# Optimization experiments

Measured on AMD Instinct MI355X. Metric: run time of the kernel, lower is better.

## Reference

```python
import jax, jax.numpy as jnp
import numpy as np

N_NODES = 20000
N_EDGES = 320000
N_GRAPHS = 32
C = 256
L = 4
IN_DIM = 739
EDGE_DIM = 2 * C + 6
LN_EPS = 1e-5


def _layernorm(x, g, b):
    mu = jnp.mean(x, axis=-1, keepdims=True)
    var = jnp.mean(jnp.square(x - mu), axis=-1, keepdims=True)
    return (x - mu) * jax.lax.rsqrt(var + LN_EPS) * g + b


def setup_inputs() -> dict:
    key = jax.random.key(0)
    ks = jax.random.split(key, 20)
    d = {}
    d["x"] = jax.random.normal(ks[0], (N_NODES, IN_DIM), jnp.float32)
    d["x_pos"] = jax.random.normal(ks[1], (N_NODES, 3), jnp.float32)
    d["edge_index"] = jax.random.randint(ks[2], (2, N_EDGES), 0, N_NODES, jnp.int32)
    d["batch"] = jnp.sort(jax.random.randint(ks[3], (N_NODES,), 0, N_GRAPHS, jnp.int32))
    s = 0.02
    d["dense_w"] = jax.random.normal(ks[4], (IN_DIM, C), jnp.float32) * s
    d["dense_b"] = jnp.zeros((C,), jnp.float32)
    d["d1_w"] = jax.random.normal(ks[5], (L, C, C), jnp.float32) * s
    d["d1_b"] = jnp.zeros((L, C), jnp.float32)
    d["ln1_g"] = jnp.ones((L, EDGE_DIM), jnp.float32)
    d["ln1_b"] = jnp.zeros((L, EDGE_DIM), jnp.float32)
    d["w1_w"] = jax.random.normal(ks[6], (L, EDGE_DIM, 4), jnp.float32) * s
    d["w1_b"] = jnp.zeros((L, 4), jnp.float32)
    d["ln2_g"] = jnp.ones((L, 4), jnp.float32)
    d["ln2_b"] = jnp.zeros((L, 4), jnp.float32)
    d["w2_w"] = jax.random.normal(ks[7], (L, 4, 1), jnp.float32) * s
    d["w2_b"] = jnp.zeros((L, 1), jnp.float32)
    d["d2_w"] = jax.random.normal(ks[8], (L, C, C), jnp.float32) * s
    d["d2_b"] = jnp.zeros((L, C), jnp.float32)
    d["head_w"] = jax.random.normal(ks[9], (C, 1), jnp.float32) * s
    d["head_b"] = jnp.zeros((1,), jnp.float32)
    return d


def reference(x, x_pos, edge_index, batch, dense_w, dense_b, d1_w, d1_b,
              ln1_g, ln1_b, w1_w, w1_b, ln2_g, ln2_b, w2_w, w2_b,
              d2_w, d2_b, head_w, head_b):
    n = x.shape[0]
    src, dst = edge_index[0], edge_index[1]
    h = x @ dense_w + dense_b  # [N, C]
    for l in range(d1_w.shape[0]):
        # message: dense1 -> GELU (dropout is identity in eval)
        m = jax.nn.gelu(h @ d1_w[l] + d1_b[l], approximate=False)  # [N, C]
        sx = m[src]                                                # [E, C]
        # edge-MLP input: [src_x, dst_x, src_pos, dst_pos]
        e = jnp.concatenate([sx, m[dst], x_pos[src], x_pos[dst]], axis=-1)  # [E, 2C+6]
        e = _layernorm(e, ln1_g[l], ln1_b[l])
        e = jax.nn.gelu(e @ w1_w[l] + w1_b[l], approximate=False)  # [E, 4]
        e = _layernorm(e, ln2_g[l], ln2_b[l])
        w = jax.nn.sigmoid(e @ w2_w[l] + w2_b[l])                  # [E, 1]
        agg = jax.ops.segment_sum(sx * w, dst, num_segments=n)     # [N, C]
        # update: dense2 -> GELU
        h = jax.nn.gelu(agg @ d2_w[l] + d2_b[l], approximate=False)
    # global mean pool over graphs
    sums = jax.ops.segment_sum(h, batch, num_segments=N_GRAPHS)           # [G, C]
    cnts = jax.ops.segment_sum(jnp.ones((n, 1), h.dtype), batch, num_segments=N_GRAPHS)
    pooled = sums / jnp.maximum(cnts, 1.0)
    return pooled @ head_w + head_b  # [G, 1]
```

## Files before the change

### kernel.cpp

```cpp
#include <hip/hip_runtime.h>
#include <math.h>

#define N_NODES 20000
#define N_EDGES 320000
#define N_GRAPHS 32
#define CDIM 256
#define IN_DIMV 739
#define KPAD_DENSE 768
#define ED_DIM 518
#define NLAYERS 4
#define LN_EPS 1e-5f
#define SCAN_BLOCKS ((N_NODES + 255) / 256)

typedef _Float16 f16x8 __attribute__((ext_vector_type(8)));
typedef _Float16 f16x4 __attribute__((ext_vector_type(4)));
typedef float f32x4 __attribute__((ext_vector_type(4)));

__device__ __forceinline__ float gelu_exact(float x) {
    return 0.5f * x * (1.f + erff(x * 0.7071067811865475f));
}

__global__ __launch_bounds__(256)
void prep_all(const float* __restrict__ ln1_g, const float* __restrict__ ln1_b,
              const float* __restrict__ w1_w, float* __restrict__ cw,
              float* __restrict__ SgSb,
              const float* __restrict__ dense_w, _Float16* __restrict__ wt_dense,
              const float* __restrict__ d1_w, const float* __restrict__ d2_w,
              _Float16* __restrict__ wt_sq, int* __restrict__ deg,
              float* __restrict__ sdot) {
    __shared__ float smem[2048 + 64];
    int b = blockIdx.x, tid = threadIdx.x;
    if (b < 79) {
        int i = b * 256 + tid;
        if (i < N_NODES) deg[i] = 0;
    } else if (b < 83) {
        int l = b - 79;
        float sg[4] = {0, 0, 0, 0}, sb[4] = {0, 0, 0, 0};
        for (int i = tid; i < ED_DIM; i += 256) {
            float g = ln1_g[l * ED_DIM + i];
            float bb = ln1_b[l * ED_DIM + i];
            float4 w = *(const float4*)&w1_w[(size_t)(l * ED_DIM + i) * 4];
            float4 c = make_float4(g * w.x, g * w.y, g * w.z, g * w.w);
            *(float4*)&cw[(size_t)(l * ED_DIM + i) * 4] = c;
            sg[0] += c.x; sg[1] += c.y; sg[2] += c.z; sg[3] += c.w;
            sb[0] += bb * w.x; sb[1] += bb * w.y; sb[2] += bb * w.z; sb[3] += bb * w.w;
        }
        for (int c = 0; c < 4; c++) { smem[tid * 8 + c] = sg[c]; smem[tid * 8 + 4 + c] = sb[c]; }
        __syncthreads();
        for (int s = 128; s > 0; s >>= 1) {
            if (tid < s)
                for (int c = 0; c < 8; c++) smem[tid * 8 + c] += smem[(tid + s) * 8 + c];
            __syncthreads();
        }
        if (tid < 8) SgSb[l * 8 + tid] = smem[tid];
    } else if (b < 275) {
        int q = b - 83;
        int kt = q >> 3, nt = q & 7;
        int i = tid >> 5, j = tid & 31;
        float* T = smem;
#pragma unroll
        for (int ii = 0; ii < 4; ii++) {
            int k = kt * 32 + i + ii * 8;
            T[(i + ii * 8) * 33 + j] = (k < IN_DIMV) ? dense_w[(size_t)k * 256 + nt * 32 + j] : 0.f;
        }
        __syncthreads();
#pragma unroll
        for (int ii = 0; ii < 4; ii++) {
            int n = nt * 32 + i + ii * 8;
            wt_dense[(size_t)n * KPAD_DENSE + kt * 32 + j] = (_Float16)T[j * 33 + i + ii * 8];
        }
    } else if (b < 787) {
        int q = b - 275;
        int z = q >> 6, kt = (q >> 3) & 7, nt = q & 7;
        const float* W = (z < 4) ? d1_w + (size_t)z * 65536 : d2_w + (size_t)(z - 4) * 65536;
        _Float16* O = wt_sq + (size_t)z * 65536;
        int i = tid >> 5, j = tid & 31;
        float* T = smem;
#pragma unroll
        for (int ii = 0; ii < 4; ii++)
            T[(i + ii * 8) * 33 + j] = W[(size_t)(kt * 32 + i + ii * 8) * 256 + nt * 32 + j];
        __syncthreads();
#pragma unroll
        for (int ii = 0; ii < 4; ii++)
            O[(size_t)(nt * 32 + i + ii * 8) * 256 + kt * 32 + j] = (_Float16)T[j * 33 + i + ii * 8];
    } else {
        int i = (b - 787) * 256 + tid;
        if (i < N_NODES) sdot[i] = 0.f;
    }
}

__global__ void hist_gstart_kernel(const int* __restrict__ ei, const int* __restrict__ batch,
                                   int* __restrict__ deg, int* __restrict__ gstart) {
    int e = blockIdx.x * 256 + threadIdx.x;
    if (e < N_EDGES) atomicAdd(&deg[ei[N_EDGES + e]], 1);
    if (e < N_NODES) {
        int b = batch[e];
        int bprev = (e == 0) ? -1 : batch[e - 1];
        for (int g = bprev + 1; g <= b; g++) gstart[g] = e;
        if (e == N_NODES - 1)
            for (int g = b + 1; g <= N_GRAPHS; g++) gstart[g] = N_NODES;
    }
}

__global__ __launch_bounds__(256)
void scan1_kernel(const int* __restrict__ deg, int* __restrict__ bsum) {
    __shared__ int red[256];
    int t = threadIdx.x;
    int i = blockIdx.x * 256 + t;
    red[t] = (i < N_NODES) ? deg[i] : 0;
    __syncthreads();
    for (int s = 128; s > 0; s >>= 1) {
        if (t < s) red[t] += red[t + s];
        __syncthreads();
    }
    if (t == 0) bsum[blockIdx.x] = red[0];
}

__global__ __launch_bounds__(128)
void scan2_kernel(const int* __restrict__ bsum, int* __restrict__ boff) {
    __shared__ int s[128];
    int t = threadIdx.x;
    int v = (t < SCAN_BLOCKS) ? bsum[t] : 0;
    s[t] = v;
    __syncthreads();
    for (int off = 1; off < 128; off <<= 1) {
        int o = (t >= off) ? s[t - off] : 0;
        __syncthreads();
        s[t] += o;
        __syncthreads();
    }
    if (t < SCAN_BLOCKS) boff[t] = s[t] - v;
}

__global__ __launch_bounds__(256)
void scan3_kernel(const int* __restrict__ deg, const int* __restrict__ boff,
                  int* __restrict__ row_start, int* __restrict__ cursor) {
    __shared__ int s[256];
    int t = threadIdx.x;
    int i = blockIdx.x * 256 + t;
    int v = (i < N_NODES) ? deg[i] : 0;
    s[t] = v;
    __syncthreads();
    for (int off = 1; off < 256; off <<= 1) {
        int o = (t >= off) ? s[t - off] : 0;
        __syncthreads();
        s[t] += o;
        __syncthreads();
    }
    int base = boff[blockIdx.x];
    int excl = base + s[t] - v;
    if (i < N_NODES) {
        row_start[i] = excl;
        cursor[i] = excl;
    }
    if (i == N_NODES - 1) row_start[N_NODES] = base + s[t];
}

__global__ void scatter_kernel(const int* __restrict__ ei, int* __restrict__ cursor,
                               int* __restrict__ csr_src, int* __restrict__ slot) {
    int e = blockIdx.x * 256 + threadIdx.x;
    if (e < N_EDGES) {
        int d = ei[N_EDGES + e];
        int pos = atomicAdd(&cursor[d], 1);
        csr_src[pos] = ei[e];
        slot[e] = pos;
    }
}

__global__ __launch_bounds__(256)
void gemm_dense(const float* __restrict__ A, const _Float16* __restrict__ Bt,
                const float* __restrict__ bias, _Float16* __restrict__ C) {
    __shared__ __align__(16) _Float16 As[32 * 72];
    __shared__ __align__(16) _Float16 Bs[128 * 72];
    int tid = threadIdx.x;
    int row0 = blockIdx.x * 32;
    int col0 = blockIdx.y * 128;
    int wave = tid >> 6, lane = tid & 63;
    int quad = lane >> 4, lrow = lane & 15;
    int wrow = wave >> 1, wcol = wave & 1;

    int ar = tid >> 3, ak8 = (tid & 7) * 8;
    int br = tid >> 1, bh = (tid & 1) * 32;

    const float* Arow = &A[(size_t)(row0 + ar) * IN_DIMV];
    const _Float16* Brow = &Bt[(size_t)(col0 + br) * KPAD_DENSE];

    const int ntiles = KPAD_DENSE >> 6;
    float a_f[8];
#pragma unroll
    for (int j = 0; j < 8; j++) {
        int gk = ak8 + j;
        a_f[j] = (gk < IN_DIMV) ? Arow[gk] : 0.f;
    }
    uint4 b_raw0 = *(const uint4*)&Brow[bh];
    uint4 b_raw1 = *(const uint4*)&Brow[bh + 8];
    uint4 b_raw2 = *(const uint4*)&Brow[bh + 16];
    uint4 b_raw3 = *(const uint4*)&Brow[bh + 24];

    f32x4 acc[4];
#pragma unroll
    for (int t = 0; t < 4; t++) acc[t] = (f32x4){0.f, 0.f, 0.f, 0.f};

    for (int kt = 0; kt < ntiles; ++kt) {
        f16x8 ah;
#pragma unroll
        for (int j = 0; j < 8; j++) ah[j] = (_Float16)a_f[j];
        *(f16x8*)&As[ar * 72 + ak8] = ah;
        *(uint4*)&Bs[br * 72 + bh] = b_raw0;
        *(uint4*)&Bs[br * 72 + bh + 8] = b_raw1;
        *(uint4*)&Bs[br * 72 + bh + 16] = b_raw2;
        *(uint4*)&Bs[br * 72 + bh + 24] = b_raw3;
        __syncthreads();

        if (kt + 1 < ntiles) {
            int k0 = (kt + 1) << 6;
#pragma unroll
            for (int j = 0; j < 8; j++) {
                int gk = k0 + ak8 + j;
                a_f[j] = (gk < IN_DIMV) ? Arow[gk] : 0.f;
            }
            b_raw0 = *(const uint4*)&Brow[k0 + bh];
            b_raw1 = *(const uint4*)&Brow[k0 + bh + 8];
            b_raw2 = *(const uint4*)&Brow[k0 + bh + 16];
            b_raw3 = *(const uint4*)&Brow[k0 + bh + 24];
        }

#pragma unroll
        for (int h = 0; h < 2; h++) {
            f16x8 af = *(const f16x8*)&As[(wrow * 16 + lrow) * 72 + h * 32 + quad * 8];
#pragma unroll
            for (int t = 0; t < 4; t++) {
                f16x8 bf = *(const f16x8*)&Bs[((wcol * 4 + t) * 16 + lrow) * 72 + h * 32 + quad * 8];
                acc[t] = __builtin_amdgcn_mfma_f32_16x16x32_f16(af, bf, acc[t], 0, 0, 0);
            }
        }
        __syncthreads();
    }

    int orow = row0 + wrow * 16 + quad * 4;
#pragma unroll
    for (int t = 0; t < 4; t++) {
        int col = col0 + (wcol * 4 + t) * 16 + lrow;
        float bv = bias[col];
#pragma unroll
        for (int r = 0; r < 4; r++)
            C[(size_t)(orow + r) * 256 + col] = (_Float16)(acc[t][r] + bv);
    }
}

template <bool GELU, bool DOT>
__global__ __launch_bounds__(256)
void gemm_mfma(const _Float16* __restrict__ A, const _Float16* __restrict__ Bt,
               const float* __restrict__ bias, _Float16* __restrict__ C,
               const float* __restrict__ head_w, float* __restrict__ sdot) {
    __shared__ __align__(16) _Float16 As[32 * 72];
    __shared__ __align__(16) _Float16 Bs[128 * 72];
    int tid = threadIdx.x;
    int row0 = blockIdx.x * 32;
    int col0 = blockIdx.y * 128;
    int wave = tid >> 6, lane = tid & 63;
    int quad = lane >> 4, lrow = lane & 15;
    int wrow = wave >> 1, wcol = wave & 1;

    int ar = tid >> 3, ak8 = (tid & 7) * 8;
    int br = tid >> 1, bh = (tid & 1) * 32;

    const _Float16* Arow = &A[(size_t)(row0 + ar) * CDIM];
    const _Float16* Brow = &Bt[(size_t)(col0 + br) * CDIM];

    const int ntiles = CDIM >> 6;
    uint4 a_raw = *(const uint4*)&Arow[ak8];
    uint4 b_raw0 = *(const uint4*)&Brow[bh];
    uint4 b_raw1 = *(const uint4*)&Brow[bh + 8];
    uint4 b_raw2 = *(const uint4*)&Brow[bh + 16];
    uint4 b_raw3 = *(const uint4*)&Brow[bh + 24];

    f32x4 acc[4];
#pragma unroll
    for (int t = 0; t < 4; t++) acc[t] = (f32x4){0.f, 0.f, 0.f, 0.f};

    for (int kt = 0; kt < ntiles; ++kt) {
        *(uint4*)&As[ar * 72 + ak8] = a_raw;
        *(uint4*)&Bs[br * 72 + bh] = b_raw0;
        *(uint4*)&Bs[br * 72 + bh + 8] = b_raw1;
        *(uint4*)&Bs[br * 72 + bh + 16] = b_raw2;
        *(uint4*)&Bs[br * 72 + bh + 24] = b_raw3;
        __syncthreads();

        if (kt + 1 < ntiles) {
            int k0 = (kt + 1) << 6;
            a_raw = *(const uint4*)&Arow[k0 + ak8];
            b_raw0 = *(const uint4*)&Brow[k0 + bh];
            b_raw1 = *(const uint4*)&Brow[k0 + bh + 8];
            b_raw2 = *(const uint4*)&Brow[k0 + bh + 16];
            b_raw3 = *(const uint4*)&Brow[k0 + bh + 24];
        }

#pragma unroll
        for (int h = 0; h < 2; h++) {
            f16x8 af = *(const f16x8*)&As[(wrow * 16 + lrow) * 72 + h * 32 + quad * 8];
#pragma unroll
            for (int t = 0; t < 4; t++) {
                f16x8 bf = *(const f16x8*)&Bs[((wcol * 4 + t) * 16 + lrow) * 72 + h * 32 + quad * 8];
                acc[t] = __builtin_amdgcn_mfma_f32_16x16x32_f16(af, bf, acc[t], 0, 0, 0);
            }
        }
        __syncthreads();
    }

    int orow = row0 + wrow * 16 + quad * 4;
    if (DOT) {
        float dp[4] = {0.f, 0.f, 0.f, 0.f};
#pragma unroll
        for (int t = 0; t < 4; t++) {
            int col = col0 + (wcol * 4 + t) * 16 + lrow;
            float hw = head_w[col];
            float bv = bias[col];
#pragma unroll
            for (int r = 0; r < 4; r++)
                dp[r] += gelu_exact(acc[t][r] + bv) * hw;
        }
#pragma unroll
        for (int r = 0; r < 4; r++) {
#pragma unroll
            for (int off = 1; off < 16; off <<= 1)
                dp[r] += __shfl_xor(dp[r], off, 64);
        }
        if (lrow == 0) {
#pragma unroll
            for (int r = 0; r < 4; r++) atomicAdd(&sdot[orow + r], dp[r]);
        }
    } else {
#pragma unroll
        for (int t = 0; t < 4; t++) {
            int col = col0 + (wcol * 4 + t) * 16 + lrow;
            float bv = bias[col];
#pragma unroll
            for (int r = 0; r < 4; r++) {
                float v = acc[t][r] + bv;
                C[(size_t)(orow + r) * 256 + col] = (_Float16)(GELU ? gelu_exact(v) : v);
            }
        }
    }
}

__global__ __launch_bounds__(256)
void node_summary_kernel(const _Float16* __restrict__ m, const float* __restrict__ cw,
                         float* __restrict__ ns) {
    __shared__ __align__(16) float4 s_cw[512];
    int tid = threadIdx.x;
    for (int i = tid; i < 512; i += 256) s_cw[i] = *(const float4*)&cw[(size_t)i * 4];
    __syncthreads();
    int n = blockIdx.x * 4 + (tid >> 6);
    if (n >= N_NODES) return;
    int lane = tid & 63;
    f16x4 a4 = *(const f16x4*)&m[(size_t)n * CDIM + lane * 4];
    float av[4] = {(float)a4[0], (float)a4[1], (float)a4[2], (float)a4[3]};
    float Q1 = 0.f, Q2 = 0.f, P1[4] = {0, 0, 0, 0}, P2[4] = {0, 0, 0, 0};
#pragma unroll
    for (int j = 0; j < 4; j++) {
        Q1 += av[j];
        Q2 += av[j] * av[j];
        float4 c0 = s_cw[lane * 4 + j];
        float4 c1 = s_cw[256 + lane * 4 + j];
        P1[0] += av[j] * c0.x; P1[1] += av[j] * c0.y; P1[2] += av[j] * c0.z; P1[3] += av[j] * c0.w;
        P2[0] += av[j] * c1.x; P2[1] += av[j] * c1.y; P2[2] += av[j] * c1.z; P2[3] += av[j] * c1.w;
    }
#pragma unroll
    for (int off = 1; off < 64; off <<= 1) {
        Q1 += __shfl_xor(Q1, off, 64);
        Q2 += __shfl_xor(Q2, off, 64);
        P1[0] += __shfl_xor(P1[0], off, 64);
        P1[1] += __shfl_xor(P1[1], off, 64);
        P1[2] += __shfl_xor(P1[2], off, 64);
        P1[3] += __shfl_xor(P1[3], off, 64);
        P2[0] += __shfl_xor(P2[0], off, 64);
        P2[1] += __shfl_xor(P2[1], off, 64);
        P2[2] += __shfl_xor(P2[2], off, 64);
        P2[3] += __shfl_xor(P2[3], off, 64);
    }
    if (lane == 0) {
        float* p = &ns[(size_t)n * 12];
        *(float4*)p = make_float4(P1[0], P1[1], P1[2], P1[3]);
        *(float4*)(p + 4) = make_float4(P2[0], P2[1], P2[2], P2[3]);
        p[8] = Q1;
        p[9] = Q2;
    }
}

__global__ __launch_bounds__(256)
void edge_weight_kernel(const float* __restrict__ ns, const float* __restrict__ x_pos,
                        const int* __restrict__ ei, const float* __restrict__ cw,
                        const float* __restrict__ SgSb, const float* __restrict__ w1_b,
                        const float* __restrict__ ln2_g, const float* __restrict__ ln2_b,
                        const float* __restrict__ w2_w, const float* __restrict__ w2_b,
                        const int* __restrict__ slot, float* __restrict__ w_csr) {
    int e = blockIdx.x * 256 + threadIdx.x;
    if (e >= N_EDGES) return;
    int s = ei[e], d = ei[N_EDGES + e];
    const float* nss = &ns[(size_t)s * 12];
    const float* nsd = &ns[(size_t)d * 12];
    float4 p1 = *(const float4*)nss;
    float4 p2 = *(const float4*)(nsd + 4);
    float S1 = nss[8] + nsd[8];
    float S2 = nss[9] + nsd[9];
    float D[4] = {p1.x + p2.x, p1.y + p2.y, p1.z + p2.z, p1.w + p2.w};
    float ps[6];
    ps[0] = x_pos[(size_t)s * 3 + 0];
    ps[1] = x_pos[(size_t)s * 3 + 1];
    ps[2] = x_pos[(size_t)s * 3 + 2];
    ps[3] = x_pos[(size_t)d * 3 + 0];
    ps[4] = x_pos[(size_t)d * 3 + 1];
    ps[5] = x_pos[(size_t)d * 3 + 2];
#pragma unroll
    for (int k = 0; k < 6; k++) {
        S1 += ps[k];
        S2 += ps[k] * ps[k];
        float4 c = *(const float4*)&cw[(size_t)(512 + k) * 4];
        D[0] += ps[k] * c.x; D[1] += ps[k] * c.y; D[2] += ps[k] * c.z; D[3] += ps[k] * c.w;
    }
    const float inv = 1.f / 518.f;
    float mu = S1 * inv;
    float var = fmaf(-mu, mu, S2 * inv);
    float rstd = rsqrtf(var + LN_EPS);
    float t[4];
#pragma unroll
    for (int c = 0; c < 4; c++)
        t[c] = gelu_exact(rstd * (D[c] - mu * SgSb[c]) + SgSb[4 + c] + w1_b[c]);
    float mu2 = 0.25f * (t[0] + t[1] + t[2] + t[3]);
    float var2 = 0.25f * ((t[0] - mu2) * (t[0] - mu2) + (t[1] - mu2) * (t[1] - mu2) +
                          (t[2] - mu2) * (t[2] - mu2) + (t[3] - mu2) * (t[3] - mu2));
    float r2 = rsqrtf(var2 + LN_EPS);
    float z = w2_b[0];
#pragma unroll
    for (int c = 0; c < 4; c++)
        z += ((t[c] - mu2) * r2 * ln2_g[c] + ln2_b[c]) * w2_w[c];
    w_csr[slot[e]] = 1.f / (1.f + expf(-z));
}

__global__ __launch_bounds__(256)
void agg_kernel(const _Float16* __restrict__ m, const int* __restrict__ csr_src,
                const float* __restrict__ w_csr, const int* __restrict__ row_start,
                _Float16* __restrict__ agg) {
    int n = blockIdx.x * 4 + (threadIdx.x >> 6);
    if (n >= N_NODES) return;
    int lane = threadIdx.x & 63;
    int beg = row_start[n], end = row_start[n + 1];
    float a0 = 0.f, a1 = 0.f, a2 = 0.f, a3 = 0.f;
    int j = beg;
    for (; j + 8 <= end; j += 8) {
        int si[8];
        float wi[8];
#pragma unroll
        for (int u = 0; u < 8; u++) { si[u] = csr_src[j + u]; wi[u] = w_csr[j + u]; }
        f16x4 v[8];
#pragma unroll
        for (int u = 0; u < 8; u++) v[u] = *(const f16x4*)&m[(size_t)si[u] * CDIM + lane * 4];
#pragma unroll
        for (int u = 0; u < 8; u++) {
            a0 = fmaf(wi[u], (float)v[u][0], a0);
            a1 = fmaf(wi[u], (float)v[u][1], a1);
            a2 = fmaf(wi[u], (float)v[u][2], a2);
            a3 = fmaf(wi[u], (float)v[u][3], a3);
        }
    }
    for (; j < end; j++) {
        int s = csr_src[j];
        float w = w_csr[j];
        f16x4 v = *(const f16x4*)&m[(size_t)s * CDIM + lane * 4];
        a0 = fmaf(w, (float)v[0], a0);
        a1 = fmaf(w, (float)v[1], a1);
        a2 = fmaf(w, (float)v[2], a2);
        a3 = fmaf(w, (float)v[3], a3);
    }
    f16x4 o;
    o[0] = (_Float16)a0; o[1] = (_Float16)a1; o[2] = (_Float16)a2; o[3] = (_Float16)a3;
    *(f16x4*)&agg[(size_t)n * CDIM + lane * 4] = o;
}

__global__ __launch_bounds__(256)
void final_head_kernel(const float* __restrict__ sdot, const int* __restrict__ gstart,
                       const float* __restrict__ head_b, float* __restrict__ out) {
    int g = blockIdx.x;
    int t = threadIdx.x;
    int beg = gstart[g], end = gstart[g + 1];
    float s = 0.f;
    for (int i = beg + t; i < end; i += 256) s += sdot[i];
    __shared__ float red[256];
    red[t] = s;
    __syncthreads();
    for (int k = 128; k > 0; k >>= 1) {
        if (t < k) red[t] += red[t + k];
        __syncthreads();
    }
    if (t == 0) out[g] = red[0] / fmaxf((float)(end - beg), 1.f) + head_b[0];
}

extern "C" void kernel_launch(void* const* d_in, const int* in_sizes, int n_in,
                              void* d_out, int out_size, void* d_ws, size_t ws_size,
                              hipStream_t stream) {
    const float* x       = (const float*)d_in[0];
    const float* x_pos   = (const float*)d_in[1];
    const int*   ei      = (const int*)d_in[2];
    const int*   batch   = (const int*)d_in[3];
    const float* dense_w = (const float*)d_in[4];
    const float* dense_b = (const float*)d_in[5];
    const float* d1_w    = (const float*)d_in[6];
    const float* d1_b    = (const float*)d_in[7];
    const float* ln1_g   = (const float*)d_in[8];
    const float* ln1_b   = (const float*)d_in[9];
    const float* w1_w    = (const float*)d_in[10];
    const float* w1_b    = (const float*)d_in[11];
    const float* ln2_g   = (const float*)d_in[12];
    const float* ln2_b   = (const float*)d_in[13];
    const float* w2_w    = (const float*)d_in[14];
    const float* w2_b    = (const float*)d_in[15];
    const float* d2_w    = (const float*)d_in[16];
    const float* d2_b    = (const float*)d_in[17];
    const float* head_w  = (const float*)d_in[18];
    const float* head_b  = (const float*)d_in[19];
    float* out = (float*)d_out;

    _Float16* hbuf0 = (_Float16*)d_ws;
    _Float16* hbuf1 = hbuf0 + (size_t)N_NODES * CDIM;
    _Float16* wt_dense = hbuf1 + (size_t)N_NODES * CDIM;
    _Float16* wt_sq    = wt_dense + (size_t)256 * KPAD_DENSE;
    float* cw    = (float*)(wt_sq + (size_t)8 * 256 * 256);
    float* SgSb  = cw + (size_t)NLAYERS * ED_DIM * 4;
    float* ns    = SgSb + NLAYERS * 8;
    float* sdot  = ns + (size_t)N_NODES * 12;
    float* w_csr = sdot + N_NODES;
    int* gstart    = (int*)(w_csr + N_EDGES);
    int* deg       = gstart + N_GRAPHS + 1;
    int* row_start = deg + N_NODES;
    int* cursor    = row_start + N_NODES + 1;
    int* csr_src   = cursor + N_NODES;
    int* slot      = csr_src + N_EDGES;
    int* bsum      = slot + N_EDGES;
    int* boff      = bsum + SCAN_BLOCKS;

    prep_all<<<866, 256, 0, stream>>>(ln1_g, ln1_b, w1_w, cw, SgSb,
                                      dense_w, wt_dense, d1_w, d2_w, wt_sq, deg, sdot);

    hist_gstart_kernel<<<(N_EDGES + 255) / 256, 256, 0, stream>>>(ei, batch, deg, gstart);
    scan1_kernel<<<SCAN_BLOCKS, 256, 0, stream>>>(deg, bsum);
    scan2_kernel<<<1, 128, 0, stream>>>(bsum, boff);
    scan3_kernel<<<SCAN_BLOCKS, 256, 0, stream>>>(deg, boff, row_start, cursor);
    scatter_kernel<<<(N_EDGES + 255) / 256, 256, 0, stream>>>(ei, cursor, csr_src, slot);

    const dim3 GGRID(N_NODES / 32, 2);
    gemm_dense<<<GGRID, 256, 0, stream>>>(x, wt_dense, dense_b, hbuf0);

    _Float16* h = hbuf0;
    _Float16* other = hbuf1;
    for (int l = 0; l < NLAYERS; l++) {
        gemm_mfma<true, false><<<GGRID, 256, 0, stream>>>(
            h, wt_sq + (size_t)l * 65536, d1_b + l * CDIM, other, nullptr, nullptr);
        node_summary_kernel<<<(N_NODES + 3) / 4, 256, 0, stream>>>(
            other, cw + (size_t)l * ED_DIM * 4, ns);
        edge_weight_kernel<<<(N_EDGES + 255) / 256, 256, 0, stream>>>(
            ns, x_pos, ei, cw + (size_t)l * ED_DIM * 4, SgSb + l * 8, w1_b + l * 4,
            ln2_g + l * 4, ln2_b + l * 4, w2_w + l * 4, w2_b + l, slot, w_csr);
        agg_kernel<<<(N_NODES + 3) / 4, 256, 0, stream>>>(other, csr_src, w_csr, row_start, h);
        if (l < NLAYERS - 1) {
            gemm_mfma<true, false><<<GGRID, 256, 0, stream>>>(
                h, wt_sq + (size_t)(4 + l) * 65536, d2_b + l * CDIM, other, nullptr, nullptr);
        } else {
            gemm_mfma<true, true><<<GGRID, 256, 0, stream>>>(
                h, wt_sq + (size_t)(4 + l) * 65536, d2_b + l * CDIM, other, head_w, sdot);
        }
        _Float16* tmp = h; h = other; other = tmp;
    }

    final_head_kernel<<<N_GRAPHS, 256, 0, stream>>>(sdot, gstart, head_b, out);
}
```

Before: 528.6 us.

## Unify GEMMs into double-buffered 64-row tile kernel with direct LDS loads

Replaces the two GEMM kernels with a single templated kernel. It uses a 64x128 output tile per block, XOR-swizzled unpadded shared memory, and double buffering, with global_load_lds moving the fp16 operands straight into LDS. The fp32 input GEMM converts A in registers while the MFMAs for the current tile run. The aim is more reuse per B tile and overlap of loads with compute, at the cost of more LDS per block and a full vmcnt wait every k-step.

```diff
diff --git a/kernel.cpp b/kernel.cpp
--- a/kernel.cpp
+++ b/kernel.cpp
@@ -18,6 +18,11 @@
 
 __device__ __forceinline__ float gelu_exact(float x) {
     return 0.5f * x * (1.f + erff(x * 0.7071067811865475f));
+}
+
+__device__ __forceinline__ void gll16(const void* g, void* l) {
+    __builtin_amdgcn_global_load_lds((const __attribute__((address_space(1))) void*)g,
+                                     (__attribute__((address_space(3))) void*)l, 16, 0, 0);
 }
 
 __global__ __launch_bounds__(256)
@@ -167,178 +172,185 @@
     }
 }
 
-__global__ __launch_bounds__(256)
-void gemm_dense(const float* __restrict__ A, const _Float16* __restrict__ Bt,
-                const float* __restrict__ bias, _Float16* __restrict__ C) {
-    __shared__ __align__(16) _Float16 As[32 * 72];
-    __shared__ __align__(16) _Float16 Bs[128 * 72];
-    int tid = threadIdx.x;
-    int row0 = blockIdx.x * 32;
-    int col0 = blockIdx.y * 128;
-    int wave = tid >> 6, lane = tid & 63;
-    int quad = lane >> 4, lrow = lane & 15;
-    int wrow = wave >> 1, wcol = wave & 1;
-
-    int ar = tid >> 3, ak8 = (tid & 7) * 8;
-    int br = tid >> 1, bh = (tid & 1) * 32;
-
-    const float* Arow = &A[(size_t)(row0 + ar) * IN_DIMV];
-    const _Float16* Brow = &Bt[(size_t)(col0 + br) * KPAD_DENSE];
-
-    const int ntiles = KPAD_DENSE >> 6;
-    float a_f[8];
-#pragma unroll
-    for (int j = 0; j < 8; j++) {
-        int gk = ak8 + j;
-        a_f[j] = (gk < IN_DIMV) ? Arow[gk] : 0.f;
-    }
-    uint4 b_raw0 = *(const uint4*)&Brow[bh];
-    uint4 b_raw1 = *(const uint4*)&Brow[bh + 8];
-    uint4 b_raw2 = *(const uint4*)&Brow[bh + 16];
-    uint4 b_raw3 = *(const uint4*)&Brow[bh + 24];
-
-    f32x4 acc[4];
-#pragma unroll
-    for (int t = 0; t < 4; t++) acc[t] = (f32x4){0.f, 0.f, 0.f, 0.f};
-
-    for (int kt = 0; kt < ntiles; ++kt) {
-        f16x8 ah;
-#pragma unroll
-        for (int j = 0; j < 8; j++) ah[j] = (_Float16)a_f[j];
-        *(f16x8*)&As[ar * 72 + ak8] = ah;
-        *(uint4*)&Bs[br * 72 + bh] = b_raw0;
-        *(uint4*)&Bs[br * 72 + bh + 8] = b_raw1;
-        *(uint4*)&Bs[br * 72 + bh + 16] = b_raw2;
-        *(uint4*)&Bs[br * 72 + bh + 24] = b_raw3;
-        __syncthreads();
-
-        if (kt + 1 < ntiles) {
-            int k0 = (kt + 1) << 6;
-#pragma unroll
-            for (int j = 0; j < 8; j++) {
-                int gk = k0 + ak8 + j;
-                a_f[j] = (gk < IN_DIMV) ? Arow[gk] : 0.f;
-            }
-            b_raw0 = *(const uint4*)&Brow[k0 + bh];
-            b_raw1 = *(const uint4*)&Brow[k0 + bh + 8];
-            b_raw2 = *(const uint4*)&Brow[k0 + bh + 16];
-            b_raw3 = *(const uint4*)&Brow[k0 + bh + 24];
-        }
-
-#pragma unroll
-        for (int h = 0; h < 2; h++) {
-            f16x8 af = *(const f16x8*)&As[(wrow * 16 + lrow) * 72 + h * 32 + quad * 8];
-#pragma unroll
-            for (int t = 0; t < 4; t++) {
-                f16x8 bf = *(const f16x8*)&Bs[((wcol * 4 + t) * 16 + lrow) * 72 + h * 32 + quad * 8];
-                acc[t] = __builtin_amdgcn_mfma_f32_16x16x32_f16(af, bf, acc[t], 0, 0, 0);
-            }
-        }
-        __syncthreads();
-    }
-
-    int orow = row0 + wrow * 16 + quad * 4;
-#pragma unroll
-    for (int t = 0; t < 4; t++) {
-        int col = col0 + (wcol * 4 + t) * 16 + lrow;
-        float bv = bias[col];
-#pragma unroll
-        for (int r = 0; r < 4; r++)
-            C[(size_t)(orow + r) * 256 + col] = (_Float16)(acc[t][r] + bv);
-    }
-}
-
-template <bool GELU, bool DOT>
-__global__ __launch_bounds__(256)
-void gemm_mfma(const _Float16* __restrict__ A, const _Float16* __restrict__ Bt,
-               const float* __restrict__ bias, _Float16* __restrict__ C,
-               const float* __restrict__ head_w, float* __restrict__ sdot) {
-    __shared__ __align__(16) _Float16 As[32 * 72];
-    __shared__ __align__(16) _Float16 Bs[128 * 72];
-    int tid = threadIdx.x;
-    int row0 = blockIdx.x * 32;
-    int col0 = blockIdx.y * 128;
-    int wave = tid >> 6, lane = tid & 63;
-    int quad = lane >> 4, lrow = lane & 15;
-    int wrow = wave >> 1, wcol = wave & 1;
-
-    int ar = tid >> 3, ak8 = (tid & 7) * 8;
-    int br = tid >> 1, bh = (tid & 1) * 32;
-
-    const _Float16* Arow = &A[(size_t)(row0 + ar) * CDIM];
-    const _Float16* Brow = &Bt[(size_t)(col0 + br) * CDIM];
-
-    const int ntiles = CDIM >> 6;
-    uint4 a_raw = *(const uint4*)&Arow[ak8];
-    uint4 b_raw0 = *(const uint4*)&Brow[bh];
-    uint4 b_raw1 = *(const uint4*)&Brow[bh + 8];
-    uint4 b_raw2 = *(const uint4*)&Brow[bh + 16];
-    uint4 b_raw3 = *(const uint4*)&Brow[bh + 24];
-
-    f32x4 acc[4];
-#pragma unroll
-    for (int t = 0; t < 4; t++) acc[t] = (f32x4){0.f, 0.f, 0.f, 0.f};
-
-    for (int kt = 0; kt < ntiles; ++kt) {
-        *(uint4*)&As[ar * 72 + ak8] = a_raw;
-        *(uint4*)&Bs[br * 72 + bh] = b_raw0;
-        *(uint4*)&Bs[br * 72 + bh + 8] = b_raw1;
-        *(uint4*)&Bs[br * 72 + bh + 16] = b_raw2;
-        *(uint4*)&Bs[br * 72 + bh + 24] = b_raw3;
-        __syncthreads();
-
-        if (kt + 1 < ntiles) {
-            int k0 = (kt + 1) << 6;
-            a_raw = *(const uint4*)&Arow[k0 + ak8];
-            b_raw0 = *(const uint4*)&Brow[k0 + bh];
-            b_raw1 = *(const uint4*)&Brow[k0 + bh + 8];
-            b_raw2 = *(const uint4*)&Brow[k0 + bh + 16];
-            b_raw3 = *(const uint4*)&Brow[k0 + bh + 24];
-        }
-
-#pragma unroll
-        for (int h = 0; h < 2; h++) {
-            f16x8 af = *(const f16x8*)&As[(wrow * 16 + lrow) * 72 + h * 32 + quad * 8];
-#pragma unroll
-            for (int t = 0; t < 4; t++) {
-                f16x8 bf = *(const f16x8*)&Bs[((wcol * 4 + t) * 16 + lrow) * 72 + h * 32 + quad * 8];
-                acc[t] = __builtin_amdgcn_mfma_f32_16x16x32_f16(af, bf, acc[t], 0, 0, 0);
-            }
-        }
-        __syncthreads();
-    }
-
-    int orow = row0 + wrow * 16 + quad * 4;
-    if (DOT) {
-        float dp[4] = {0.f, 0.f, 0.f, 0.f};
-#pragma unroll
-        for (int t = 0; t < 4; t++) {
-            int col = col0 + (wcol * 4 + t) * 16 + lrow;
-            float hw = head_w[col];
-            float bv = bias[col];
-#pragma unroll
-            for (int r = 0; r < 4; r++)
-                dp[r] += gelu_exact(acc[t][r] + bv) * hw;
-        }
-#pragma unroll
-        for (int r = 0; r < 4; r++) {
-#pragma unroll
-            for (int off = 1; off < 16; off <<= 1)
-                dp[r] += __shfl_xor(dp[r], off, 64);
+template <int KSTEPS, int AK, bool AFP32, bool GELU_ACT, bool DOT>
+__global__ __launch_bounds__(256)
+void gemm_v2(const void* __restrict__ Av, const _Float16* __restrict__ Bt,
+             const float* __restrict__ bias, _Float16* __restrict__ C,
+             const float* __restrict__ head_w, float* __restrict__ sdot) {
+    constexpr int BSTR = KSTEPS * 64;
+    __shared__ __align__(16) _Float16 As[2][64 * 64];
+    __shared__ __align__(16) _Float16 Bs[2][128 * 64];
+
+    const int tid = threadIdx.x;
+    const int row0 = blockIdx.x * 64;
+    const int col0 = blockIdx.y * 128;
+    const int wave = tid >> 6, lane = tid & 63;
+    const int quad = lane >> 4, lrow = lane & 15;
+    const int wrow = wave >> 1, wcol = wave & 1;
+
+    const int sr = tid >> 3;
+    const int scb = (tid & 7) << 4;
+    const int srcCb = scb ^ ((sr & 7) << 4);
+
+    const char* bsrc[4];
+#pragma unroll
+    for (int i = 0; i < 4; ++i)
+        bsrc[i] = (const char*)Bt + (size_t)(col0 + i * 32 + sr) * (BSTR * 2) + srcCb;
+    char* const bdst = (char*)&Bs[0][0] + tid * 16;
+
+    const char* asrc[2];
+    const float* afsrc[2];
+    char* const adst = (char*)&As[0][0] + tid * 16;
+    char* const adstw = (char*)&As[0][0] + sr * 128 + srcCb;
+#pragma unroll
+    for (int i = 0; i < 2; ++i) {
+        int ar = row0 + i * 32 + sr;
+        ar = (ar < N_NODES) ? ar : (N_NODES - 1);
+        asrc[i] = (const char*)Av + (size_t)ar * (AK * 2) + srcCb;
+        afsrc[i] = (const float*)Av + (size_t)ar * AK + (scb >> 1);
+    }
+
+    const int swz = ((lrow & 7) << 4) ^ (quad << 4);
+    const int aro0 = (wrow * 32 + lrow) * 128;
+    const int aro1 = aro0 + 2048;
+    int bro[4];
+#pragma unroll
+    for (int t = 0; t < 4; ++t) bro[t] = (wcol * 64 + t * 16 + lrow) * 128;
+
+    f32x4 acc[2][4];
+#pragma unroll
+    for (int i = 0; i < 2; ++i)
+#pragma unroll
+        for (int t = 0; t < 4; ++t) acc[i][t] = (f32x4){0.f, 0.f, 0.f, 0.f};
+
+    {
+        float av0[8], av1[8];
+        if constexpr (AFP32) {
+            if constexpr (64 <= AK) {
+#pragma unroll
+                for (int j = 0; j < 8; ++j) { av0[j] = afsrc[0][j]; av1[j] = afsrc[1][j]; }
+            }
+        }
+#pragma unroll
+        for (int i = 0; i < 4; ++i) gll16(bsrc[i], bdst + i * 4096);
+        if constexpr (!AFP32) {
+#pragma unroll
+            for (int i = 0; i < 2; ++i) gll16(asrc[i], adst + i * 4096);
+        } else {
+            f16x8 v0, v1;
+#pragma unroll
+            for (int j = 0; j < 8; ++j) { v0[j] = (_Float16)av0[j]; v1[j] = (_Float16)av1[j]; }
+            *(f16x8*)(adstw) = v0;
+            *(f16x8*)(adstw + 4096) = v1;
+        }
+    }
+    asm volatile("s_waitcnt vmcnt(0)" ::: "memory");
+    __syncthreads();
+
+    int cur = 0;
+    for (int kt = 0; kt < KSTEPS; ++kt) {
+        const bool more = (kt + 1 < KSTEPS);
+        float av0[8], av1[8];
+        if (more) {
+            const int kbyte = (kt + 1) * 128;
+            if constexpr (AFP32) {
+                const int k0 = (kt + 1) * 64;
+                if ((kt + 2) * 64 <= AK) {
+#pragma unroll
+                    for (int j = 0; j < 8; ++j) { av0[j] = afsrc[0][k0 + j]; av1[j] = afsrc[1][k0 + j]; }
+                } else {
+                    const int kbase = k0 + (scb >> 1);
+#pragma unroll
+                    for (int j = 0; j < 8; ++j) {
+                        av0[j] = (kbase + j < AK) ? afsrc[0][k0 + j] : 0.f;
+                        av1[j] = (kbase + j < AK) ? afsrc[1][k0 + j] : 0.f;
+                    }
+                }
+            }
+            const int bb = (cur ^ 1) * 16384;
+#pragma unroll
+            for (int i = 0; i < 4; ++i) gll16(bsrc[i] + kbyte, bdst + bb + i * 4096);
+            if constexpr (!AFP32) {
+                const int ab = (cur ^ 1) * 8192;
+#pragma unroll
+                for (int i = 0; i < 2; ++i) gll16(asrc[i] + kbyte, adst + ab + i * 4096);
+            }
+        }
+
+        const char* pa = (const char*)&As[0][0] + cur * 8192;
+        const char* pb = (const char*)&Bs[0][0] + cur * 16384;
+#pragma unroll
+        for (int h = 0; h < 2; ++h) {
+            const int cbs = (h << 6) ^ swz;
+            f16x8 af0 = *(const f16x8*)(pa + aro0 + cbs);
+            f16x8 af1 = *(const f16x8*)(pa + aro1 + cbs);
+#pragma unroll
+            for (int t = 0; t < 4; ++t) {
+                f16x8 bf = *(const f16x8*)(pb + bro[t] + cbs);
+                acc[0][t] = __builtin_amdgcn_mfma_f32_16x16x32_f16(af0, bf, acc[0][t], 0, 0, 0);
+                acc[1][t] = __builtin_amdgcn_mfma_f32_16x16x32_f16(af1, bf, acc[1][t], 0, 0, 0);
+            }
+        }
+
+        if constexpr (AFP32) {
+            if (more) {
+                const int ab = (cur ^ 1) * 8192;
+                f16x8 v0, v1;
+#pragma unroll
+                for (int j = 0; j < 8; ++j) { v0[j] = (_Float16)av0[j]; v1[j] = (_Float16)av1[j]; }
+                *(f16x8*)(adstw + ab) = v0;
+                *(f16x8*)(adstw + ab + 4096) = v1;
+            }
+        }
+        asm volatile("s_waitcnt vmcnt(0)" ::: "memory");
+        __syncthreads();
+        cur ^= 1;
+    }
+
+    const int orow = row0 + wrow * 32 + quad * 4;
+    const int ocolb = col0 + wcol * 64 + lrow;
+    if constexpr (DOT) {
+        float dp0[4] = {0.f, 0.f, 0.f, 0.f}, dp1[4] = {0.f, 0.f, 0.f, 0.f};
+#pragma unroll
+        for (int t = 0; t < 4; ++t) {
+            const int col = ocolb + t * 16;
+            const float hw = head_w[col];
+            const float bv = bias[col];
+#pragma unroll
+            for (int r = 0; r < 4; ++r) {
+                dp0[r] += gelu_exact(acc[0][t][r] + bv) * hw;
+                dp1[r] += gelu_exact(acc[1][t][r] + bv) * hw;
+            }
+        }
+#pragma unroll
+        for (int r = 0; r < 4; ++r) {
+#pragma unroll
+            for (int off = 1; off < 16; off <<= 1) {
+                dp0[r] += __shfl_xor(dp0[r], off, 64);
+                dp1[r] += __shfl_xor(dp1[r], off, 64);
+            }
         }
         if (lrow == 0) {
 #pragma unroll
-            for (int r = 0; r < 4; r++) atomicAdd(&sdot[orow + r], dp[r]);
+            for (int r = 0; r < 4; ++r) {
+                if (orow + r < N_NODES) atomicAdd(&sdot[orow + r], dp0[r]);
+                if (orow + 16 + r < N_NODES) atomicAdd(&sdot[orow + 16 + r], dp1[r]);
+            }
         }
     } else {
 #pragma unroll
-        for (int t = 0; t < 4; t++) {
-            int col = col0 + (wcol * 4 + t) * 16 + lrow;
-            float bv = bias[col];
-#pragma unroll
-            for (int r = 0; r < 4; r++) {
-                float v = acc[t][r] + bv;
-                C[(size_t)(orow + r) * 256 + col] = (_Float16)(GELU ? gelu_exact(v) : v);
+        for (int t = 0; t < 4; ++t) {
+            const int col = ocolb + t * 16;
+            const float bv = bias[col];
+#pragma unroll
+            for (int r = 0; r < 4; ++r) {
+                float v0 = acc[0][t][r] + bv;
+                float v1 = acc[1][t][r] + bv;
+                if constexpr (GELU_ACT) { v0 = gelu_exact(v0); v1 = gelu_exact(v1); }
+                if (orow + r < N_NODES)
+                    C[(size_t)(orow + r) * 256 + col] = (_Float16)v0;
+                if (orow + 16 + r < N_NODES)
+                    C[(size_t)(orow + 16 + r) * 256 + col] = (_Float16)v1;
             }
         }
     }
@@ -548,13 +560,14 @@
     scan3_kernel<<<SCAN_BLOCKS, 256, 0, stream>>>(deg, boff, row_start, cursor);
     scatter_kernel<<<(N_EDGES + 255) / 256, 256, 0, stream>>>(ei, cursor, csr_src, slot);
 
-    const dim3 GGRID(N_NODES / 32, 2);
-    gemm_dense<<<GGRID, 256, 0, stream>>>(x, wt_dense, dense_b, hbuf0);
+    const dim3 G2((N_NODES + 63) / 64, 2);
+    gemm_v2<12, IN_DIMV, true, false, false><<<G2, 256, 0, stream>>>(
+        x, wt_dense, dense_b, hbuf0, nullptr, nullptr);
 
     _Float16* h = hbuf0;
     _Float16* other = hbuf1;
     for (int l = 0; l < NLAYERS; l++) {
-        gemm_mfma<true, false><<<GGRID, 256, 0, stream>>>(
+        gemm_v2<4, CDIM, false, true, false><<<G2, 256, 0, stream>>>(
             h, wt_sq + (size_t)l * 65536, d1_b + l * CDIM, other, nullptr, nullptr);
         node_summary_kernel<<<(N_NODES + 3) / 4, 256, 0, stream>>>(
             other, cw + (size_t)l * ED_DIM * 4, ns);
@@ -563,10 +576,10 @@
             ln2_g + l * 4, ln2_b + l * 4, w2_w + l * 4, w2_b + l, slot, w_csr);
         agg_kernel<<<(N_NODES + 3) / 4, 256, 0, stream>>>(other, csr_src, w_csr, row_start, h);
         if (l < NLAYERS - 1) {
-            gemm_mfma<true, false><<<GGRID, 256, 0, stream>>>(
+            gemm_v2<4, CDIM, false, true, false><<<G2, 256, 0, stream>>>(
                 h, wt_sq + (size_t)(4 + l) * 65536, d2_b + l * CDIM, other, nullptr, nullptr);
         } else {
-            gemm_mfma<true, true><<<GGRID, 256, 0, stream>>>(
+            gemm_v2<4, CDIM, false, true, true><<<G2, 256, 0, stream>>>(
                 h, wt_sq + (size_t)(4 + l) * 65536, d2_b + l * CDIM, other, head_w, sdot);
         }
         _Float16* tmp = h; h = other; other = tmp;
```

Result: faster. 507.8 us (-3.9%).
